# Optimization experiments

Measured on AMD Instinct MI355X. Metric: run time of the kernel, lower is better.

Reference implementation:

```python
import jax, jax.numpy as jnp
import numpy as np

N = 50000      # nodes
E = 800000     # edges (avg degree 16)
IN = 128       # input feature dim
D = 128        # embed dim (heads=1, concat)
SLOPE = 0.2    # GATv2Conv default negative_slope


def setup_inputs() -> dict:
    key = jax.random.key(0)
    ks = jax.random.split(key, 16)
    s_in = 1.0 / np.sqrt(IN)
    s_d = 1.0 / np.sqrt(D)
    inp = {
        "node_fts": jax.random.normal(ks[0], (N, IN), dtype=jnp.float32),
        "edge_index": jax.random.randint(ks[1], (2, E), 0, N, dtype=jnp.int64),
        # layer 1 (in_dim -> embed_dim)
        "Wl1": jax.random.normal(ks[2], (IN, D), dtype=jnp.float32) * s_in,
        "bl1": jnp.zeros((D,), dtype=jnp.float32),
        "Wr1": jax.random.normal(ks[3], (IN, D), dtype=jnp.float32) * s_in,
        "br1": jnp.zeros((D,), dtype=jnp.float32),
        "att1": jax.random.normal(ks[4], (D,), dtype=jnp.float32) * s_d,
        "bias1": jnp.zeros((D,), dtype=jnp.float32),
        # layer 2 (embed_dim -> embed_dim)
        "Wl2": jax.random.normal(ks[5], (D, D), dtype=jnp.float32) * s_d,
        "bl2": jnp.zeros((D,), dtype=jnp.float32),
        "Wr2": jax.random.normal(ks[6], (D, D), dtype=jnp.float32) * s_d,
        "br2": jnp.zeros((D,), dtype=jnp.float32),
        "att2": jax.random.normal(ks[7], (D,), dtype=jnp.float32) * s_d,
        "bias2": jnp.zeros((D,), dtype=jnp.float32),
    }
    return inp


def gatv2_layer(x, src, dst, Wl, bl, Wr, br, att, bias):
    # GATv2Conv (heads=1, share_weights=False):
    #   x_j (source message features) = lin_l(x), x_i (target) = lin_r(x)
    xl = x @ Wl + bl                                      # [N, D]
    xr = x @ Wr + br                                      # [N, D]
    e = jax.nn.leaky_relu(xl[src] + xr[dst], SLOPE)       # [E, D]
    logits = e @ att                                      # [E]
    # softmax over incoming edges of each target node
    m = jax.ops.segment_max(logits, dst, num_segments=N)  # [N], -inf for isolated
    m = jnp.where(jnp.isneginf(m), 0.0, m)
    a = jnp.exp(logits - m[dst])                          # [E]
    s = jax.ops.segment_sum(a, dst, num_segments=N)       # [N]
    a = a / jnp.maximum(s[dst], 1e-16)
    out = jax.ops.segment_sum(a[:, None] * xl[src], dst, num_segments=N)  # [N, D]
    return out + bias


def reference(node_fts, edge_index,
              Wl1, bl1, Wr1, br1, att1, bias1,
              Wl2, bl2, Wr2, br2, att2, bias2):
    src, dst = edge_index[0], edge_index[1]
    x = jax.nn.relu(gatv2_layer(node_fts, src, dst, Wl1, bl1, Wr1, br1, att1, bias1))
    x = jax.nn.relu(gatv2_layer(x, src, dst, Wl2, bl2, Wr2, br2, att2, bias2))
    return x
```

## Files before the change

### kernel.cpp

```cpp
#include <hip/hip_runtime.h>
#include <hip/hip_bf16.h>
#include <hip/hip_fp16.h>

#define N_NODES 50000
#define N_EDGES 800000
#define DIM 128
#define NGROUPS (N_NODES / 16)
#define KBUCKET 196
#define BCAP 5120
#define EPB 2000
#define OSTR 260
#define TSTR 132

typedef __attribute__((ext_vector_type(8))) _Float16 hfrag8;
typedef __attribute__((ext_vector_type(4))) float f32x4;
typedef _Float16 h2 __attribute__((ext_vector_type(2)));

__device__ __forceinline__ h2 u2h(uint u){ union{uint u; h2 h;} c; c.u = u; return c.h; }

__device__ __forceinline__ float rowsum16(float p) {
  union { float f; int i; } a, b;
  a.f = p;
  b.i = __builtin_amdgcn_update_dpp(0, a.i, 0x128, 0xF, 0xF, true); a.f += b.f;
  b.i = __builtin_amdgcn_update_dpp(0, a.i, 0x124, 0xF, 0xF, true); a.f += b.f;
  b.i = __builtin_amdgcn_update_dpp(0, a.i, 0x122, 0xF, 0xF, true); a.f += b.f;
  b.i = __builtin_amdgcn_update_dpp(0, a.i, 0x121, 0xF, 0xF, true); a.f += b.f;
  return a.f;
}


__global__ __launch_bounds__(256) void bucket_scatter_k(
    const int* __restrict__ src, const int* __restrict__ dst,
    int* __restrict__ bucket_cnt, uint* __restrict__ bucketdata)
{
  __shared__ int cnt[KBUCKET], base[KBUCKET], cur[KBUCKET];
  int tid = threadIdx.x;
  for (int t = tid; t < KBUCKET; t += 256) { cnt[t] = 0; cur[t] = 0; }
  __syncthreads();
  int e0 = blockIdx.x * EPB;
  int dreg[8];
  #pragma unroll
  for (int it = 0; it < 8; it++) {
    int i = it*256 + tid;
    dreg[it] = (i < EPB) ? dst[e0 + i] : -1;
    if (i < EPB) atomicAdd(&cnt[dreg[it] >> 8], 1);
  }
  __syncthreads();
  for (int t = tid; t < KBUCKET; t += 256)
    base[t] = atomicAdd(&bucket_cnt[t], cnt[t]);
  __syncthreads();
  #pragma unroll
  for (int it = 0; it < 8; it++) {
    int i = it*256 + tid;
    if (i < EPB) {
      int s = src[e0 + i], d = dreg[it];
      int b = d >> 8;
      int r = atomicAdd(&cur[b], 1);
      bucketdata[(size_t)b * BCAP + base[b] + r] = ((uint)s << 8) | (uint)(d & 255);
    }
  }
}

__global__ __launch_bounds__(64) void prep_w(
    const float* __restrict__ Wl1, const float* __restrict__ Wr1,
    const float* __restrict__ Wl2, const float* __restrict__ Wr2,
    _Float16* __restrict__ wb, int* __restrict__ bucket_cnt)
{
  int bid = blockIdx.x;
  if (bid == 0) {
    for (int t = threadIdx.x; t < KBUCKET; t += 64) bucket_cnt[t] = 0;
  }
  int layer = bid >> 6, rest = bid & 63;
  int C = rest >> 4, g = rest & 15;
  int lane = threadIdx.x;
  int m = lane & 15, q = lane >> 4;
  int dim = g*16 + m;
  const float* W = layer ? (dim < 128 ? Wl2 : Wr2) : (dim < 128 ? Wl1 : Wr1);
  int dcol = dim & 127;
  _Float16 h[8];
  #pragma unroll
  for (int j = 0; j < 8; j++) {
    int k = C*32 + q*8 + j;
    h[j] = (_Float16)W[(size_t)k*DIM + dcol];
  }
  size_t off = ((size_t)bid*64 + lane)*8;
  *(hfrag8*)(wb + off) = *(hfrag8*)h;
}

__global__ __launch_bounds__(256) void gemm1_csr_k(
    const float* __restrict__ x, const _Float16* __restrict__ wb,
    const float* __restrict__ bl, const float* __restrict__ br,
    __half* __restrict__ xlh, __half* __restrict__ xrh,
    const int* __restrict__ bucket_cnt, const uint* __restrict__ bucketdata,
    int* __restrict__ row_start, int* __restrict__ csr_soff)
{
  __shared__ int hist[256], cur[256];
  __shared__ int wsumA[4], wsumB[4];
  __shared__ _Float16 wstage[16*64*8];
  __shared__ ushort touts[4][16*TSTR];
  int tid = threadIdx.x;

  if (blockIdx.x < KBUCKET) {
    int b = blockIdx.x;
    int lane = tid & 63, w = tid >> 6;
    int vv = (tid < b) ? bucket_cnt[tid] : 0;
    #pragma unroll
    for (int off = 32; off > 0; off >>= 1) vv += __shfl_xor(vv, off, 64);
    if (lane == 0) wsumA[w] = vv;
    hist[tid] = 0;
    __syncthreads();
    int base_csr = wsumA[0] + wsumA[1] + wsumA[2] + wsumA[3];
    int cnt = bucket_cnt[b];
    int node0 = b << 8;
    const uint* bd = bucketdata + (size_t)b * BCAP;
    for (int i = tid; i < cnt; i += 256)
      atomicAdd(&hist[bd[i] & 255], 1);
    __syncthreads();
    int v = hist[tid];
    int inc = v;
    #pragma unroll
    for (int off = 1; off < 64; off <<= 1) {
      int y = __shfl_up(inc, off, 64);
      if (lane >= off) inc += y;
    }
    if (lane == 63) wsumB[w] = inc;
    __syncthreads();
    int wpre = 0;
    #pragma unroll
    for (int i = 0; i < 4; i++) if (i < w) wpre += wsumB[i];
    int excl = wpre + inc - v;
    int node = node0 + tid;
    if (node < N_NODES) row_start[node] = base_csr + excl;
    if (b == 0 && tid == 0) row_start[N_NODES] = N_EDGES;
    cur[tid] = excl;
    __syncthreads();
    for (int i = tid; i < cnt; i += 256) {
      uint p = bd[i];
      int r = atomicAdd(&cur[p & 255], 1);
      csr_soff[base_csr + r] = (int)(p & 0xFFFFFF00u);
    }
    return;
  }

  int wv = tid >> 6, lane = tid & 63;
  int G = (blockIdx.x - KBUCKET) * 4 + wv;
  bool wvalid = (G < NGROUPS);
  if (!wvalid) G = NGROUPS - 1;

  int m = lane & 15, q = lane >> 4;
  const float* xrow = x + (size_t)(G*16 + m)*DIM + q*8;

  f32x4 acc[16];
  #pragma unroll
  for (int g = 0; g < 16; g++) acc[g] = (f32x4)(0.f);

  #pragma unroll 1
  for (int C = 0; C < 4; C++) {
    __syncthreads();
    {
      const uint4* srcw = (const uint4*)(wb + (size_t)C*16*64*8);
      uint4* dstw = (uint4*)wstage;
      #pragma unroll
      for (int k = 0; k < 4; k++)
        dstw[k*256 + tid] = srcw[k*256 + tid];
    }
    __syncthreads();
    float v[8];
    *(float4*)(v)     = *(const float4*)(xrow + C*32);
    *(float4*)(v + 4) = *(const float4*)(xrow + C*32 + 4);
    _Float16 hh[8];
    #pragma unroll
    for (int j = 0; j < 8; j++) hh[j] = (_Float16)v[j];
    hfrag8 ah = *(hfrag8*)hh;
    #pragma unroll
    for (int g = 0; g < 16; g++) {
      hfrag8 bh = *(const hfrag8*)(wstage + ((size_t)g*64 + lane)*8);
      acc[g] = __builtin_amdgcn_mfma_f32_16x16x32_f16(ah, bh, acc[g], 0, 0, 0);
    }
  }

  ushort* tw = touts[wv];
  #pragma unroll
  for (int half = 0; half < 2; half++) {
    const float* B = half ? br : bl;
    ushort* outh = half ? (ushort*)xrh : (ushort*)xlh;
    #pragma unroll
    for (int g = 0; g < 8; g++) {
      float bv = B[g*16 + m];
      #pragma unroll
      for (int r = 0; r < 4; r++) {
        __half hv = __float2half_rn(acc[half*8 + g][r] + bv);
        tw[(q*4 + r)*TSTR + g*16 + m] = *(ushort*)&hv;
      }
    }
    #pragma unroll
    for (int i = 0; i < 4; i++) {
      int c = i*64 + lane;
      int row = c >> 4, off = c & 15;
      uint4 vv = *(const uint4*)((const char*)tw + row*(TSTR*2) + off*16);
      if (wvalid)
        *(uint4*)(outh + (size_t)(G*16 + row)*DIM + off*8) = vv;
    }
  }
}


#define GAT_IDX(OFF, TBASE)                                             \
  do {                                                                  \
    if ((TBASE) < 32) {                                                 \
      int _src = ((TBASE) < 16) ? my0 : my1;                            \
      _Pragma("unroll")                                                 \
      for (int j = 0; j < 4; j++)                                       \
        OFF[j] = __builtin_amdgcn_ds_bpermute(                          \
                     grpb4 + ((((TBASE) + j) & 15) << 2), _src);        \
    } else {                                                            \
      _Pragma("unroll")                                                 \
      for (int j = 0; j < 4; j++)                                       \
        OFF[j] = csr_soff[min(r0 + (TBASE) + j, last)];                 \
    }                                                                   \
  } while (0)

#define GAT_LDR4(OFF, RAW)                                              \
  _Pragma("unroll")                                                     \
  for (int j = 0; j < 4; j++)                                           \
    RAW[j] = *(const uint4*)(xb + (size_t)(uint)OFF[j]);

#define GAT_BODY(RAW, WEXPR)                                            \
  _Pragma("unroll")                                                     \
  for (int j = 0; j < 4; j++) {                                         \
    h2 v01 = u2h(RAW[j].x), v23 = u2h(RAW[j].y);                        \
    h2 v45 = u2h(RAW[j].z), v67 = u2h(RAW[j].w);                        \
    h2 s01 = v01 + xr01, s23 = v23 + xr23;                              \
    h2 s45 = v45 + xr45, s67 = v67 + xr67;                              \
    s01 = __builtin_elementwise_max(s01, s01 * c02);                    \
    s23 = __builtin_elementwise_max(s23, s23 * c02);                    \
    s45 = __builtin_elementwise_max(s45, s45 * c02);                    \
    s67 = __builtin_elementwise_max(s67, s67 * c02);                    \
    float pA = __builtin_amdgcn_fdot2(s01, a01, 0.f, false);            \
    pA = __builtin_amdgcn_fdot2(s23, a23, pA, false);                   \
    float pB = __builtin_amdgcn_fdot2(s45, a45, 0.f, false);            \
    pB = __builtin_amdgcn_fdot2(s67, a67, pB, false);                   \
    float p = rowsum16(pA + pB);                                        \
    float w = (WEXPR);                                                  \
    l += w;                                                             \
    b0a = fmaf(w, (float)v01.x, b0a); b1a = fmaf(w, (float)v01.y, b1a); \
    b2a = fmaf(w, (float)v23.x, b2a); b3a = fmaf(w, (float)v23.y, b3a); \
    b4a = fmaf(w, (float)v45.x, b4a); b5a = fmaf(w, (float)v45.y, b5a); \
    b6a = fmaf(w, (float)v67.x, b6a); b7a = fmaf(w, (float)v67.y, b7a); \
  }

__device__ __forceinline__ void gather_core(
    int node, int lane,
    const __half* __restrict__ xlh, const __half* __restrict__ xrh,
    const int* __restrict__ row_start, const int* __restrict__ csr_soff,
    const float* __restrict__ att, const float* __restrict__ bias,
    float4& o0, float4& o1)
{
  int hl = lane & 15;
  int grpb4 = (lane & 48) << 2;
  int r0 = row_start[node];
  int deg = row_start[node + 1] - r0;
  int last = r0 + deg - 1;

  int my0 = 0, my1 = 0;
  if (deg > 0)  my0 = csr_soff[min(r0 + hl,      last)];
  if (deg > 16) my1 = csr_soff[min(r0 + 16 + hl, last)];

  uint4 rx = *(const uint4*)((const ushort*)xrh + (size_t)node*DIM + hl*8);
  h2 xr01 = u2h(rx.x), xr23 = u2h(rx.y), xr45 = u2h(rx.z), xr67 = u2h(rx.w);
  const float* ap = att + hl*8;
  float4 af0 = *(const float4*)(ap);
  float4 af1 = *(const float4*)(ap + 4);
  const float L2E = 1.44269504088896f;
  h2 a01 = {(_Float16)(af0.x*L2E), (_Float16)(af0.y*L2E)};
  h2 a23 = {(_Float16)(af0.z*L2E), (_Float16)(af0.w*L2E)};
  h2 a45 = {(_Float16)(af1.x*L2E), (_Float16)(af1.y*L2E)};
  h2 a67 = {(_Float16)(af1.z*L2E), (_Float16)(af1.w*L2E)};
  const h2 c02 = {(_Float16)0.2f, (_Float16)0.2f};

  float l = 0.f;
  float b0a=0,b1a=0,b2a=0,b3a=0,b4a=0,b5a=0,b6a=0,b7a=0;
  const char* xb = (const char*)xlh + hl*16;

  int offA[4]; uint4 rawA[4];
  int offB[4]; uint4 rawB[4];
  int nfull = deg & ~3;

  if (nfull > 0) { GAT_IDX(offA, 0); GAT_LDR4(offA, rawA); }
  #pragma unroll 1
  for (int t = 0; t < nfull; t += 8) {
    bool hasB = (t + 4 < nfull);
    if (hasB) { GAT_IDX(offB, t + 4); GAT_LDR4(offB, rawB); }
    GAT_BODY(rawA, exp2f(p));
    if (t + 8 < nfull) { GAT_IDX(offA, t + 8); GAT_LDR4(offA, rawA); }
    if (hasB) GAT_BODY(rawB, exp2f(p));
  }
  int rem = deg - nfull;
  if (rem > 0) {
    #pragma unroll
    for (int j = 0; j < 4; j++)
      offA[j] = csr_soff[min(r0 + nfull + j, last)];
    GAT_LDR4(offA, rawA);
    GAT_BODY(rawA, (j < rem) ? exp2f(p) : 0.f);
  }

  float inv = 1.f / fmaxf(l, 1e-16f);
  const float* bp = bias + hl*8;
  float4 c0 = *(const float4*)(bp);
  float4 c1 = *(const float4*)(bp + 4);
  o0.x = fmaxf(fmaf(b0a, inv, c0.x), 0.f);
  o0.y = fmaxf(fmaf(b1a, inv, c0.y), 0.f);
  o0.z = fmaxf(fmaf(b2a, inv, c0.z), 0.f);
  o0.w = fmaxf(fmaf(b3a, inv, c0.w), 0.f);
  o1.x = fmaxf(fmaf(b4a, inv, c1.x), 0.f);
  o1.y = fmaxf(fmaf(b5a, inv, c1.y), 0.f);
  o1.z = fmaxf(fmaf(b6a, inv, c1.z), 0.f);
  o1.w = fmaxf(fmaf(b7a, inv, c1.w), 0.f);
}

__global__ __launch_bounds__(256) void fused_g1_gemm2_k(
    const __half* __restrict__ xlh, const __half* __restrict__ xrh,
    const int* __restrict__ row_start, const int* __restrict__ csr_soff,
    const float* __restrict__ att, const float* __restrict__ bias,
    const _Float16* __restrict__ wb2,
    const float* __restrict__ bl2, const float* __restrict__ br2,
    __half* __restrict__ xlh2, __half* __restrict__ xrh2)
{
  __shared__ ushort xs[16*128];
  __shared__ ushort outs[16*OSTR];
  int tid = threadIdx.x;
  int wv = tid >> 6, lane = tid & 63;
  int q4 = lane >> 4, hl = lane & 15;
  int nl = wv*4 + q4;
  int base = blockIdx.x * 16;

  float4 o0, o1;
  gather_core(base + nl, lane, xlh, xrh, row_start, csr_soff, att, bias, o0, o1);
  __half2 p0 = __floats2half2_rn(o0.x, o0.y);
  __half2 p1 = __floats2half2_rn(o0.z, o0.w);
  __half2 p2 = __floats2half2_rn(o1.x, o1.y);
  __half2 p3 = __floats2half2_rn(o1.z, o1.w);
  uint4 pk = make_uint4(*(uint*)&p0, *(uint*)&p1, *(uint*)&p2, *(uint*)&p3);
  *(uint4*)((char*)xs + nl*256 + ((hl*16) ^ ((nl&7)<<4))) = pk;
  __syncthreads();

  int m = lane & 15, q = lane >> 4;
  f32x4 acc[4];
  #pragma unroll
  for (int g = 0; g < 4; g++) acc[g] = (f32x4)(0.f);
  #pragma unroll
  for (int C = 0; C < 4; C++) {
    hfrag8 ah = *(const hfrag8*)((const char*)xs + m*256 + ((C*64 + q*16) ^ ((m&7)<<4)));
    #pragma unroll
    for (int g = 0; g < 4; g++) {
      int gg = wv*4 + g;
      size_t boff = ((size_t)(C*16 + gg)*64 + lane)*8;
      hfrag8 bh = *(const hfrag8*)(wb2 + boff);
      acc[g] = __builtin_amdgcn_mfma_f32_16x16x32_f16(ah, bh, acc[g], 0, 0, 0);
    }
  }
  #pragma unroll
  for (int g = 0; g < 4; g++) {
    int gg = wv*4 + g;
    int dim = gg*16 + m;
    float bv = (gg < 8) ? bl2[dim] : br2[dim - 128];
    #pragma unroll
    for (int r = 0; r < 4; r++) {
      int row = q*4 + r;
      __half hv = __float2half_rn(acc[g][r] + bv);
      outs[row*OSTR + gg*16 + m] = *(ushort*)&hv;
    }
  }
  __syncthreads();
  #pragma unroll
  for (int p = 0; p < 2; p++) {
    int c = p*256 + tid;
    int row = c >> 5, off = c & 31;
    uint4 v = *(const uint4*)((const char*)outs + row*(OSTR*2) + off*16);
    int nodeo = base + row;
    int d0 = off*8;
    ushort* dstp = (d0 < 128) ? ((ushort*)xlh2 + (size_t)nodeo*DIM + d0)
                              : ((ushort*)xrh2 + (size_t)nodeo*DIM + (d0 - 128));
    *(uint4*)dstp = v;
  }
}

__global__ __launch_bounds__(256) void gat_gather2(
    const __half* __restrict__ xlh, const __half* __restrict__ xrh,
    const int* __restrict__ row_start, const int* __restrict__ csr_soff,
    const float* __restrict__ att, const float* __restrict__ bias,
    float* __restrict__ outf)
{
  int wave = (blockIdx.x * 256 + threadIdx.x) >> 6;
  int lane = threadIdx.x & 63;
  int q4 = lane >> 4;
  int hl = lane & 15;
  int node = wave * 4 + q4;
  float4 o0, o1;
  gather_core(node, lane, xlh, xrh, row_start, csr_soff, att, bias, o0, o1);
  float* op = outf + (size_t)node*DIM + hl*8;
  *(float4*)(op)     = o0;
  *(float4*)(op + 4) = o1;
}

extern "C" void kernel_launch(void* const* d_in, const int* in_sizes, int n_in,
                              void* d_out, int out_size, void* d_ws, size_t ws_size,
                              hipStream_t stream)
{
  const float* node_fts = (const float*)d_in[0];
  const int*  edge_index = (const int*)d_in[1];
  const float* Wl1 = (const float*)d_in[2];
  const float* bl1 = (const float*)d_in[3];
  const float* Wr1 = (const float*)d_in[4];
  const float* br1 = (const float*)d_in[5];
  const float* att1 = (const float*)d_in[6];
  const float* bias1 = (const float*)d_in[7];
  const float* Wl2 = (const float*)d_in[8];
  const float* bl2 = (const float*)d_in[9];
  const float* Wr2 = (const float*)d_in[10];
  const float* br2 = (const float*)d_in[11];
  const float* att2 = (const float*)d_in[12];
  const float* bias2 = (const float*)d_in[13];
  const int* src = edge_index;
  const int* dst = edge_index + N_EDGES;

  char* ws = (char*)d_ws;
  __half* xlh = (__half*)ws;               ws += (size_t)N_NODES*DIM*2;
  __half* xrh = (__half*)ws;               ws += (size_t)N_NODES*DIM*2;
  __half* xlh2 = (__half*)ws;              ws += (size_t)N_NODES*DIM*2;
  __half* xrh2 = (__half*)ws;              ws += (size_t)N_NODES*DIM*2;
  _Float16* wb = (_Float16*)ws;            ws += 2*4*16*64*8*2;
  int* row_start   = (int*)ws;             ws += (N_NODES+1)*4;
  int* csr_soff    = (int*)ws;             ws += (size_t)N_EDGES*4;
  int* bucket_cnt  = (int*)ws;             ws += KBUCKET*4;
  uint* bucketdata = (uint*)ws;            ws += (size_t)KBUCKET*BCAP*4;

  const int W_LAYER = 4*16*64*8;

  int gemm_blocks = (NGROUPS + 3) / 4;
  int gather_blocks = N_NODES / 16;

  prep_w<<<128, 64, 0, stream>>>(Wl1, Wr1, Wl2, Wr2, wb, bucket_cnt);
  bucket_scatter_k<<<N_EDGES/EPB, 256, 0, stream>>>(src, dst, bucket_cnt, bucketdata);
  gemm1_csr_k<<<KBUCKET + gemm_blocks, 256, 0, stream>>>(
      node_fts, wb, bl1, br1, xlh, xrh,
      bucket_cnt, bucketdata, row_start, csr_soff);
  fused_g1_gemm2_k<<<gather_blocks, 256, 0, stream>>>(
      xlh, xrh, row_start, csr_soff, att1, bias1,
      wb + W_LAYER, bl2, br2, xlh2, xrh2);
  gat_gather2<<<gather_blocks, 256, 0, stream>>>(
      xlh2, xrh2, row_start, csr_soff, att2, bias2, (float*)d_out);
}
```

Before: 214.7 us.

## Stage bucket scatter in LDS for coalesced writes; alias weight stage onto output tile

The bucket scatter kernel now sorts each block's edge payloads by bucket in shared memory, using a wave prefix scan over bucket counts, and then writes them out contiguously per bucket. The previous version wrote directly to scattered global addresses. The bucket id is packed into the top byte so the write pass can recover the destination offset, which assumes source ids fit in 16 bits. Separately, the GEMM kernel reuses the output transpose buffer as the weight staging area to cut shared memory use and raise occupancy. This costs one extra barrier before the outputs are written.

```diff
diff --git a/kernel.cpp b/kernel.cpp
--- a/kernel.cpp
+++ b/kernel.cpp
@@ -33,10 +33,15 @@
     const int* __restrict__ src, const int* __restrict__ dst,
     int* __restrict__ bucket_cnt, uint* __restrict__ bucketdata)
 {
-  __shared__ int cnt[KBUCKET], base[KBUCKET], cur[KBUCKET];
+  __shared__ int cnt[KBUCKET], cur[KBUCKET];
+  __shared__ int lofs[KBUCKET], gbase[KBUCKET];
+  __shared__ int wsum[4];
+  __shared__ uint spay[EPB];
   int tid = threadIdx.x;
+  int lane = tid & 63, w = tid >> 6;
   for (int t = tid; t < KBUCKET; t += 256) { cnt[t] = 0; cur[t] = 0; }
   __syncthreads();
+
   int e0 = blockIdx.x * EPB;
   int dreg[8];
   #pragma unroll
@@ -46,9 +51,25 @@
     if (i < EPB) atomicAdd(&cnt[dreg[it] >> 8], 1);
   }
   __syncthreads();
-  for (int t = tid; t < KBUCKET; t += 256)
-    base[t] = atomicAdd(&bucket_cnt[t], cnt[t]);
-  __syncthreads();
+
+  int v = (tid < KBUCKET) ? cnt[tid] : 0;
+  int inc = v;
+  #pragma unroll
+  for (int off = 1; off < 64; off <<= 1) {
+    int y = __shfl_up(inc, off, 64);
+    if (lane >= off) inc += y;
+  }
+  if (lane == 63) wsum[w] = inc;
+  __syncthreads();
+  int wpre = 0;
+  #pragma unroll
+  for (int i = 0; i < 4; i++) if (i < w) wpre += wsum[i];
+  if (tid < KBUCKET) {
+    lofs[tid]  = wpre + inc - v;
+    gbase[tid] = atomicAdd(&bucket_cnt[tid], v);
+  }
+  __syncthreads();
+
   #pragma unroll
   for (int it = 0; it < 8; it++) {
     int i = it*256 + tid;
@@ -56,7 +77,19 @@
       int s = src[e0 + i], d = dreg[it];
       int b = d >> 8;
       int r = atomicAdd(&cur[b], 1);
-      bucketdata[(size_t)b * BCAP + base[b] + r] = ((uint)s << 8) | (uint)(d & 255);
+      spay[lofs[b] + r] = ((uint)b << 24) | ((uint)s << 8) | (uint)(d & 255);
+    }
+  }
+  __syncthreads();
+
+  #pragma unroll
+  for (int it = 0; it < 8; it++) {
+    int i = it*256 + tid;
+    if (i < EPB) {
+      uint e = spay[i];
+      int b = (int)(e >> 24);
+      int pos = gbase[b] + (i - lofs[b]);
+      bucketdata[(size_t)b * BCAP + pos] = e & 0x00FFFFFFu;
     }
   }
 }
@@ -96,8 +129,7 @@
 {
   __shared__ int hist[256], cur[256];
   __shared__ int wsumA[4], wsumB[4];
-  __shared__ _Float16 wstage[16*64*8];
-  __shared__ ushort touts[4][16*TSTR];
+  __shared__ __align__(16) ushort touts[4][16*TSTR];
   int tid = threadIdx.x;
 
   if (blockIdx.x < KBUCKET) {
@@ -147,6 +179,7 @@
   bool wvalid = (G < NGROUPS);
   if (!wvalid) G = NGROUPS - 1;
 
+  _Float16* wstage = (_Float16*)&touts[0][0];
   int m = lane & 15, q = lane >> 4;
   const float* xrow = x + (size_t)(G*16 + m)*DIM + q*8;
 
@@ -178,6 +211,7 @@
       acc[g] = __builtin_amdgcn_mfma_f32_16x16x32_f16(ah, bh, acc[g], 0, 0, 0);
     }
   }
+  __syncthreads();
 
   ushort* tw = touts[wv];
   #pragma unroll
```

Result: no change. 214.5 us (-0.1%).
